# Kernel optimization log

Hardware: AMD Instinct MI355X
Metric: run time of the kernel (lower is better)

Reference implementation:

```python
import jax, jax.numpy as jnp
import numpy as np

B, C, H, W = 8, 512, 64, 64
RED = 4
CR = C // RED  # 128

def setup_inputs() -> dict:
    key = jax.random.key(0)
    k1, k2, k3 = jax.random.split(key, 3)
    x = jax.random.normal(k1, (B, C, H, W), dtype=jnp.float32)
    # conv_in: 1x1 conv, no bias -> weight [3*CR, C]
    w_in = jax.random.normal(k2, (3 * CR, C), dtype=jnp.float32) * 0.02
    # conv_out: 1x1 conv, no bias -> weight [C, CR]
    w_out = jax.random.normal(k3, (C, CR), dtype=jnp.float32) * 0.02
    return {"x": x, "w_in": w_in, "w_out": w_out}

def reference(x, w_in, w_out):
    b, c, h, w = x.shape
    n = h * w
    xf = x.reshape(b, c, n)                         # flatten spatial -> [B,C,N]
    proj = jnp.einsum('oc,bcn->bon', w_in, xf)      # 1x1 conv_in -> [B,3*CR,N]
    emb_a, emb_b, g = jnp.split(proj, 3, axis=1)    # each [B,CR,N]
    # unscaled full self-attention over N spatial tokens
    weights = jnp.einsum('bcn,bcm->bnm', emb_a, emb_b)   # [B,N,N]
    weights = jax.nn.softmax(weights, axis=2)
    y = jnp.einsum('bnm,bcm->bnc', weights, g)           # [B,N,CR]
    y = jnp.einsum('oc,bnc->bon', w_out, y)              # 1x1 conv_out -> [B,C,N]
    return x + y.reshape(b, c, h, w)
```

## Files before the change

### kernel.cpp

```cpp
#include <hip/hip_runtime.h>


typedef __attribute__((ext_vector_type(8))) short short8;
typedef __attribute__((ext_vector_type(4))) float f32x4;
typedef __attribute__((ext_vector_type(16))) float f32x16;

__device__ inline unsigned bfr(float f) {
  union { float f; unsigned u; } v; v.f = f;
  return v.u + 0x8000u;
}
__device__ inline unsigned short f2bf(float f) { return (unsigned short)(bfr(f) >> 16); }
__device__ inline unsigned pack2(float a, float b) {
  return __builtin_amdgcn_perm(bfr(b), bfr(a), 0x07060302u);
}
__device__ inline int sw(int row, int col, int stride_halves) {
  return row * stride_halves + ((((col >> 3) ^ (row & 7)) << 3) | (col & 7));
}
__device__ inline void load_lds16(const void* g, void* l) {
  __builtin_amdgcn_global_load_lds(
      (const __attribute__((address_space(1))) unsigned int*)g,
      (__attribute__((address_space(3))) unsigned int*)l, 16, 0, 0);
}

__global__ __launch_bounds__(256) void k_prep(const float* __restrict__ w_in,
                                              const float* __restrict__ w_out,
                                              unsigned short* __restrict__ wi,
                                              unsigned short* __restrict__ wo) {
  int i = blockIdx.x * 256 + threadIdx.x;
  const float* src;
  unsigned short* dst;
  int base;
  if (i < 24576) { src = w_in;  dst = wi; base = i * 8; }
  else           { src = w_out; dst = wo; base = (i - 24576) * 8; }
  float4 d0 = *(const float4*)&src[base];
  float4 d1 = *(const float4*)&src[base + 4];
  uint4 p;
  p.x = pack2(d0.x, d0.y); p.y = pack2(d0.z, d0.w);
  p.z = pack2(d1.x, d1.y); p.w = pack2(d1.z, d1.w);
  *(uint4*)&dst[base] = p;
}

__global__ __launch_bounds__(256) void k_proj(const float* __restrict__ x,
                                              const unsigned short* __restrict__ wi,
                                              unsigned short* __restrict__ ab,
                                              unsigned short* __restrict__ gC) {
  __shared__ unsigned short A_lds[128 * 64];
  __shared__ unsigned short B_lds[64 * 64];
  const int t = threadIdx.x;
  const int lane = t & 63;
  const int w = t >> 6;
  const int l15 = lane & 15;
  const int quad = lane >> 4;
  const int n0 = blockIdx.x * 64;
  const int o0 = blockIdx.y * 128;
  const int b = blockIdx.z;
  const int ch8g = t >> 5;
  const int tp = t & 31;

  f32x4 acc[2][4];
#pragma unroll
  for (int i = 0; i < 2; i++)
#pragma unroll
    for (int j = 0; j < 4; j++) acc[i][j] = (f32x4)0.f;

  for (int k0 = 0; k0 < 512; k0 += 64) {
#pragma unroll
    for (int j = 0; j < 4; j++) {
      int row = w * 32 + j * 8 + (lane >> 3);
      int gs = (lane & 7) ^ (row & 7);
      load_lds16(&wi[(size_t)(o0 + row) * 512 + k0 + gs * 8],
                 (void*)&A_lds[(w * 32 + j * 8) * 64]);
    }
    {
      float2 d[8];
#pragma unroll
      for (int j = 0; j < 8; j++)
        d[j] = *(const float2*)&x[((size_t)(b * 512 + k0 + ch8g * 8 + j)) * 4096 + n0 + tp * 2];
#pragma unroll
      for (int i = 0; i < 2; i++) {
        int r = tp * 2 + i;
        uint4 pv;
        if (i == 0) {
          pv.x = pack2(d[0].x, d[1].x); pv.y = pack2(d[2].x, d[3].x);
          pv.z = pack2(d[4].x, d[5].x); pv.w = pack2(d[6].x, d[7].x);
        } else {
          pv.x = pack2(d[0].y, d[1].y); pv.y = pack2(d[2].y, d[3].y);
          pv.z = pack2(d[4].y, d[5].y); pv.w = pack2(d[6].y, d[7].y);
        }
        *(uint4*)&B_lds[sw(r, ch8g * 8, 64)] = pv;
      }
    }
    __syncthreads();
#pragma unroll
    for (int kk = 0; kk < 64; kk += 32) {
      short8 a0 = *(const short8*)&A_lds[sw(w * 32 + l15, kk + quad * 8, 64)];
      short8 a1 = *(const short8*)&A_lds[sw(w * 32 + 16 + l15, kk + quad * 8, 64)];
#pragma unroll
      for (int ns = 0; ns < 4; ns++) {
        short8 bb = *(const short8*)&B_lds[sw(ns * 16 + l15, kk + quad * 8, 64)];
        acc[0][ns] = __builtin_amdgcn_mfma_f32_16x16x32_bf16(a0, bb, acc[0][ns], 0, 0, 0);
        acc[1][ns] = __builtin_amdgcn_mfma_f32_16x16x32_bf16(a1, bb, acc[1][ns], 0, 0, 0);
      }
    }
    __syncthreads();
  }
  if (o0 < 256) {
#pragma unroll
    for (int ms = 0; ms < 2; ms++) {
      int o = o0 + w * 32 + ms * 16 + quad * 4;
#pragma unroll
      for (int ns = 0; ns < 4; ns++) {
        int n = n0 + ns * 16 + l15;
        uint2 p;
        p.x = pack2(acc[ms][ns][0], acc[ms][ns][1]);
        p.y = pack2(acc[ms][ns][2], acc[ms][ns][3]);
        *(uint2*)&ab[((size_t)(b * 4096 + n)) * 256 + o] = p;
      }
    }
  } else {
#pragma unroll
    for (int ms = 0; ms < 2; ms++) {
      int og = w * 32 + ms * 16 + quad * 4;
#pragma unroll
      for (int ns = 0; ns < 4; ns++) {
        int n = n0 + ns * 16 + l15;
#pragma unroll
        for (int r = 0; r < 4; r++)
          gC[((size_t)(b * 128 + og + r)) * 4096 + n] = f2bf(acc[ms][ns][r]);
      }
    }
  }
}

__global__ __launch_bounds__(256, 2) void k_attn(const unsigned short* __restrict__ ab,
                                                 const unsigned short* __restrict__ gC,
                                                 unsigned short* __restrict__ yt) {
  __shared__ uint4 smem4[65536 / 16];
  unsigned short* smem_h = (unsigned short*)smem4;
  float* Obuf = (float*)smem4;
  float* lsumbuf = (float*)((char*)smem4 + 33024);
  unsigned* Pbuf = (unsigned*)((char*)smem4 + 33280);

  const int t = threadIdx.x;
  const int lane = t & 63;
  const int w = t >> 6;
  const int wr = w & 1;
  const int wc = w >> 1;
  const int l31 = lane & 31;
  const int h = lane >> 5;
  const int l7 = l31 & 7;
  const int q0 = blockIdx.x * 64;
  const int b = blockIdx.y;

  short8 qf[8];
  {
    const unsigned short* qp = &ab[((size_t)(b * 4096 + q0 + wc * 32 + l31)) * 256 + h * 8];
#pragma unroll
    for (int ks = 0; ks < 8; ks++) qf[ks] = *(const short8*)&qp[ks * 16];
  }

  const int krow_c = w * 16 + (lane >> 4);
  const int vrow_c = w * 32 + (lane >> 3);

  auto dma_tile = [&](int kt, int buf) {
    unsigned short* Kb = smem_h + buf * 8192;
    unsigned short* Vb = smem_h + 16384 + buf * 8192;
#pragma unroll
    for (int j = 0; j < 4; j++) {
      int row = krow_c + j * 4;
      int gs = (lane & 15) ^ (row & 7);
      load_lds16(&ab[((size_t)(b * 4096 + kt + row)) * 256 + 128 + gs * 8],
                 (void*)&Kb[(w * 16 + j * 4) * 128]);
    }
#pragma unroll
    for (int j = 0; j < 4; j++) {
      int row = vrow_c + j * 8;
      int gs = (lane & 7) ^ (row & 7);
      load_lds16(&gC[((size_t)(b * 128 + row)) * 4096 + kt + gs * 8],
                 (void*)&Vb[(w * 32 + j * 8) * 64]);
    }
  };

  f32x16 O[4];
#pragma unroll
  for (int i = 0; i < 4; i++) O[i] = (f32x16)0.f;
  float lsum = 0.f;
  const int rowK = wr * 32 + l31;

  dma_tile(0, 0);
  __syncthreads();

  for (int it = 0; it < 64; ++it) {
    if (it < 63) dma_tile((it + 1) * 64, (it + 1) & 1);
    const unsigned short* Kc = smem_h + (it & 1) * 8192;
    const unsigned short* Vc = smem_h + 16384 + (it & 1) * 8192;

    f32x16 accS = (f32x16)0.f;
#pragma unroll
    for (int ks = 0; ks < 8; ks++) {
      short8 ak = *(const short8*)&Kc[rowK * 128 + (((ks * 2 + h) ^ l7) << 3)];
      accS = __builtin_amdgcn_mfma_f32_32x32x16_bf16(ak, qf[ks], accS, 0, 0, 0);
    }

    float ps[16];
#pragma unroll
    for (int r = 0; r < 16; r++) {
      ps[r] = __expf(accS[r]);
      lsum += ps[r];
    }
    unsigned u[8];
#pragma unroll
    for (int i = 0; i < 8; i++) u[i] = pack2(ps[2 * i], ps[2 * i + 1]);

    short8 pfrag[2];
#pragma unroll
    for (int f = 0; f < 2; f++) {
      unsigned a0 = u[4 * f + 0], a1 = u[4 * f + 1], a2 = u[4 * f + 2], a3 = u[4 * f + 3];
      unsigned r0 = __shfl_xor(h ? a0 : a2, 32);
      unsigned r1 = __shfl_xor(h ? a1 : a3, 32);
      union { unsigned uu[4]; short8 s; } cv;
      if (h == 0) { cv.uu[0] = a0; cv.uu[1] = a1; cv.uu[2] = r0; cv.uu[3] = r1; }
      else        { cv.uu[0] = r0; cv.uu[1] = r1; cv.uu[2] = a2; cv.uu[3] = a3; }
      pfrag[f] = cv.s;
    }

#pragma unroll
    for (int ct = 0; ct < 4; ct++) {
      int rowV = ct * 32 + l31;
#pragma unroll
      for (int f = 0; f < 2; f++) {
        short8 av = *(const short8*)&Vc[rowV * 64 + (((wr * 4 + f * 2 + h) ^ l7) << 3)];
        O[ct] = __builtin_amdgcn_mfma_f32_32x32x16_bf16(av, pfrag[f], O[ct], 0, 0, 0);
      }
    }
    __syncthreads();
  }

  lsum += __shfl_xor(lsum, 32);
  const int q = wc * 32 + l31;
  if (wr == 0) {
#pragma unroll
    for (int ct = 0; ct < 4; ct++)
#pragma unroll
      for (int r = 0; r < 16; r++) {
        int c = ct * 32 + (r & 3) + 8 * (r >> 2) + 4 * h;
        Obuf[q * 129 + c] = O[ct][r];
      }
    if (h == 0) lsumbuf[q] = lsum;
  }
  __syncthreads();
  if (wr == 1) {
    float linv = 1.f / (lsum + lsumbuf[q]);
#pragma unroll
    for (int ct = 0; ct < 4; ct++)
#pragma unroll
      for (int r = 0; r < 16; r += 2) {
        int c = ct * 32 + (r & 3) + 8 * (r >> 2) + 4 * h;
        float v0 = (Obuf[q * 129 + c] + O[ct][r]) * linv;
        float v1 = (Obuf[q * 129 + c + 1] + O[ct][r + 1]) * linv;
        Pbuf[q * 65 + (c >> 1)] = pack2(v0, v1);
      }
  }
  __syncthreads();
  {
    int qq = t >> 2, seg = t & 3;
    unsigned* yrow = (unsigned*)&yt[((size_t)(b * 4096 + q0 + qq)) * 128];
#pragma unroll
    for (int i = 0; i < 4; i++) {
      uint4 v;
      v.x = Pbuf[qq * 65 + seg * 16 + i * 4 + 0];
      v.y = Pbuf[qq * 65 + seg * 16 + i * 4 + 1];
      v.z = Pbuf[qq * 65 + seg * 16 + i * 4 + 2];
      v.w = Pbuf[qq * 65 + seg * 16 + i * 4 + 3];
      *(uint4*)&yrow[seg * 16 + i * 4] = v;
    }
  }
}

__global__ __launch_bounds__(256) void k_out(const float* __restrict__ x,
                                             const unsigned short* __restrict__ wo,
                                             const unsigned short* __restrict__ yt,
                                             float* __restrict__ out) {
  __shared__ unsigned short A_lds[128 * 128];
  __shared__ unsigned short B_lds[64 * 128];
  const int t = threadIdx.x;
  const int lane = t & 63;
  const int w = t >> 6;
  const int l15 = lane & 15;
  const int quad = lane >> 4;
  const int n0 = blockIdx.x * 64;
  const int o0 = blockIdx.y * 128;
  const int b = blockIdx.z;

#pragma unroll
  for (int j = 0; j < 8; j++) {
    int row = w * 32 + j * 4 + (lane >> 4);
    int gs = (lane & 15) ^ (row & 7);
    load_lds16(&wo[(size_t)(o0 + row) * 128 + gs * 8],
               (void*)&A_lds[(w * 32 + j * 4) * 128]);
  }
#pragma unroll
  for (int j = 0; j < 4; j++) {
    int row = w * 16 + j * 4 + (lane >> 4);
    int gs = (lane & 15) ^ (row & 7);
    load_lds16(&yt[((size_t)(b * 4096 + n0 + row)) * 128 + gs * 8],
               (void*)&B_lds[(w * 16 + j * 4) * 128]);
  }
  __syncthreads();

  f32x4 acc[2][4];
#pragma unroll
  for (int i = 0; i < 2; i++)
#pragma unroll
    for (int j = 0; j < 4; j++) acc[i][j] = (f32x4)0.f;
#pragma unroll
  for (int ks = 0; ks < 4; ks++) {
    short8 a0 = *(const short8*)&A_lds[sw(w * 32 + l15, ks * 32 + quad * 8, 128)];
    short8 a1 = *(const short8*)&A_lds[sw(w * 32 + 16 + l15, ks * 32 + quad * 8, 128)];
#pragma unroll
    for (int ns = 0; ns < 4; ns++) {
      short8 bb = *(const short8*)&B_lds[sw(ns * 16 + l15, ks * 32 + quad * 8, 128)];
      acc[0][ns] = __builtin_amdgcn_mfma_f32_16x16x32_bf16(a0, bb, acc[0][ns], 0, 0, 0);
      acc[1][ns] = __builtin_amdgcn_mfma_f32_16x16x32_bf16(a1, bb, acc[1][ns], 0, 0, 0);
    }
  }
#pragma unroll
  for (int ms = 0; ms < 2; ms++) {
    int o = o0 + w * 32 + ms * 16 + quad * 4;
#pragma unroll
    for (int ns = 0; ns < 4; ns++) {
      int n = n0 + ns * 16 + l15;
#pragma unroll
      for (int r = 0; r < 4; r++) {
        size_t off = ((size_t)(b * 512 + o + r)) * 4096 + n;
        out[off] = x[off] + acc[ms][ns][r];
      }
    }
  }
}

extern "C" void kernel_launch(void* const* d_in, const int* in_sizes, int n_in,
                              void* d_out, int out_size, void* d_ws, size_t ws_size,
                              hipStream_t stream) {
  const float* x = (const float*)d_in[0];
  const float* w_in = (const float*)d_in[1];
  const float* w_out = (const float*)d_in[2];
  float* out = (float*)d_out;

  unsigned short* ab = (unsigned short*)d_ws;
  unsigned short* gC = ab + (size_t)8 * 4096 * 256;
  unsigned short* yt = gC + (size_t)8 * 128 * 4096;
  unsigned short* wi = yt + (size_t)8 * 4096 * 128;
  unsigned short* wo = wi + (size_t)384 * 512;

  k_prep<<<128, 256, 0, stream>>>(w_in, w_out, wi, wo);
  k_proj<<<dim3(64, 3, 8), 256, 0, stream>>>(x, wi, ab, gC);
  k_attn<<<dim3(64, 8), 256, 0, stream>>>(ab, gC, yt);
  k_out<<<dim3(64, 4, 8), 256, 0, stream>>>(x, wo, yt, out);
}
```

Before: 235.6 us.

## Pre-transpose x to bf16 token-major and pipeline projection GEMM with LDS DMA

Adds a kernel that converts x to bf16 and transposes it to [B,N,C]. The projection GEMM can then stream both operands with global_load_lds into double-buffered swizzled LDS tiles and use 32x32x16 MFMA. The goal is to drop the per-tile fp32 load, convert and transpose work inside the projection kernel and to overlap loads with compute. In exchange there is an extra kernel launch and an extra 32 MB round trip through memory. The old path is kept as a fallback when the workspace is too small.

New measurement: 250.0 us. 1.06x slower.

```diff
diff --git a/kernel.cpp b/kernel.cpp
--- a/kernel.cpp
+++ b/kernel.cpp
@@ -40,10 +40,132 @@
   *(uint4*)&dst[base] = p;
 }
 
-__global__ __launch_bounds__(256) void k_proj(const float* __restrict__ x,
+__global__ __launch_bounds__(256) void k_xpose(const float* __restrict__ x,
+                                               unsigned short* __restrict__ xbf) {
+  __shared__ unsigned short T[64 * 64];
+  const int t = threadIdx.x;
+  const int n0 = blockIdx.x * 64;
+  const int c0 = blockIdx.y * 64;
+  const int b = blockIdx.z;
+
+  float4 d[4];
+#pragma unroll
+  for (int j = 0; j < 4; j++) {
+    int c = c0 + (t >> 4) * 4 + j;
+    d[j] = *(const float4*)&x[((size_t)(b * 512 + c)) * 4096 + n0 + (t & 15) * 4];
+  }
+  const float* dp = (const float*)d;
+#pragma unroll
+  for (int i = 0; i < 4; i++) {
+    int n_loc = (t & 15) * 4 + i;
+    int c_loc = (t >> 4) * 4;
+    uint2 pv;
+    pv.x = pack2(dp[0 * 4 + i], dp[1 * 4 + i]);
+    pv.y = pack2(dp[2 * 4 + i], dp[3 * 4 + i]);
+    int pg = (c_loc >> 3) ^ ((n_loc >> 2) & 7);
+    *(uint2*)&T[n_loc * 64 + (pg << 3) + (c_loc & 7)] = pv;
+  }
+  __syncthreads();
+  {
+    int n = t >> 2, s = t & 3;
+    int x7 = (n >> 2) & 7;
+    uint4 lo = *(const uint4*)&T[n * 64 + (((2 * s + 0) ^ x7) << 3)];
+    uint4 hi = *(const uint4*)&T[n * 64 + (((2 * s + 1) ^ x7) << 3)];
+    unsigned short* dst = &xbf[((size_t)(b * 4096 + n0 + n)) * 512 + c0 + s * 16];
+    *(uint4*)&dst[0] = lo;
+    *(uint4*)&dst[8] = hi;
+  }
+}
+
+__global__ __launch_bounds__(256) void k_proj(const unsigned short* __restrict__ xbf,
                                               const unsigned short* __restrict__ wi,
                                               unsigned short* __restrict__ ab,
                                               unsigned short* __restrict__ gC) {
+  __shared__ unsigned short Abuf[2][128 * 64];
+  __shared__ unsigned short Bbuf[2][64 * 64];
+  const int t = threadIdx.x;
+  const int lane = t & 63;
+  const int w = t >> 6;
+  const int l31 = lane & 31;
+  const int h = lane >> 5;
+  const int n0 = blockIdx.x * 64;
+  const int o0 = blockIdx.y * 128;
+  const int b = blockIdx.z;
+
+  const int arow = w * 32 + (lane >> 3);
+  const int brow = w * 16 + (lane >> 3);
+
+  auto dma_tile = [&](int k0, int buf) {
+#pragma unroll
+    for (int j = 0; j < 4; j++) {
+      int row = arow + j * 8;
+      int gs = (lane & 7) ^ (row & 7);
+      load_lds16(&wi[(size_t)(o0 + row) * 512 + k0 + gs * 8],
+                 (void*)&Abuf[buf][(w * 32 + j * 8) * 64]);
+    }
+#pragma unroll
+    for (int j = 0; j < 2; j++) {
+      int row = brow + j * 8;
+      int gs = (lane & 7) ^ (row & 7);
+      load_lds16(&xbf[((size_t)(b * 4096 + n0 + row)) * 512 + k0 + gs * 8],
+                 (void*)&Bbuf[buf][(w * 16 + j * 8) * 64]);
+    }
+  };
+
+  f32x16 acc[2];
+  acc[0] = (f32x16)0.f;
+  acc[1] = (f32x16)0.f;
+
+  dma_tile(0, 0);
+  __syncthreads();
+
+  for (int it = 0; it < 8; ++it) {
+    if (it < 7) dma_tile((it + 1) * 64, (it + 1) & 1);
+    const unsigned short* A = Abuf[it & 1];
+    const unsigned short* Bm = Bbuf[it & 1];
+    short8 af[4];
+#pragma unroll
+    for (int ks = 0; ks < 4; ks++)
+      af[ks] = *(const short8*)&A[sw(w * 32 + l31, ks * 16 + h * 8, 64)];
+#pragma unroll
+    for (int nt = 0; nt < 2; nt++) {
+#pragma unroll
+      for (int ks = 0; ks < 4; ks++) {
+        short8 bf = *(const short8*)&Bm[sw(nt * 32 + l31, ks * 16 + h * 8, 64)];
+        acc[nt] = __builtin_amdgcn_mfma_f32_32x32x16_bf16(af[ks], bf, acc[nt], 0, 0, 0);
+      }
+    }
+    __syncthreads();
+  }
+
+  if (o0 < 256) {
+#pragma unroll
+    for (int nt = 0; nt < 2; nt++) {
+      int n = n0 + nt * 32 + l31;
+#pragma unroll
+      for (int r = 0; r < 16; r += 2) {
+        int o = o0 + w * 32 + (r & 3) + 8 * (r >> 2) + 4 * h;
+        *(unsigned*)&ab[((size_t)(b * 4096 + n)) * 256 + o] =
+            pack2(acc[nt][r], acc[nt][r + 1]);
+      }
+    }
+  } else {
+#pragma unroll
+    for (int nt = 0; nt < 2; nt++) {
+      int n = n0 + nt * 32 + l31;
+#pragma unroll
+      for (int r = 0; r < 16; r++) {
+        int c = w * 32 + (r & 3) + 8 * (r >> 2) + 4 * h;
+        gC[((size_t)(b * 128 + c)) * 4096 + n] = f2bf(acc[nt][r]);
+      }
+    }
+  }
+}
+
+__global__ __launch_bounds__(256) void k_proj_inline(const float* __restrict__ x,
+                                                     const unsigned short* __restrict__ wi,
+                                                     unsigned short* __restrict__ ab,
+                                                     unsigned short* __restrict__ gC) {
   __shared__ unsigned short A_lds[128 * 64];
   __shared__ unsigned short B_lds[64 * 64];
   const int t = threadIdx.x;
@@ -349,12 +471,22 @@
 
   unsigned short* ab = (unsigned short*)d_ws;
   unsigned short* gC = ab + (size_t)8 * 4096 * 256;
-  unsigned short* yt = gC + (size_t)8 * 128 * 4096;
-  unsigned short* wi = yt + (size_t)8 * 4096 * 128;
+  unsigned short* wi = gC + (size_t)8 * 128 * 4096;
   unsigned short* wo = wi + (size_t)384 * 512;
+  unsigned short* xbf = wo + (size_t)512 * 128;
+  const size_t need_big = (size_t)(8388608 + 4194304 + 196608 + 65536 + 16777216) * 2;
 
   k_prep<<<128, 256, 0, stream>>>(w_in, w_out, wi, wo);
-  k_proj<<<dim3(64, 3, 8), 256, 0, stream>>>(x, wi, ab, gC);
-  k_attn<<<dim3(64, 8), 256, 0, stream>>>(ab, gC, yt);
-  k_out<<<dim3(64, 4, 8), 256, 0, stream>>>(x, wo, yt, out);
-}
+  if (ws_size >= need_big) {
+    unsigned short* yt = xbf;
+    k_xpose<<<dim3(64, 8, 8), 256, 0, stream>>>(x, xbf);
+    k_proj<<<dim3(64, 3, 8), 256, 0, stream>>>(xbf, wi, ab, gC);
+    k_attn<<<dim3(64, 8), 256, 0, stream>>>(ab, gC, yt);
+    k_out<<<dim3(64, 4, 8), 256, 0, stream>>>(x, wo, yt, out);
+  } else {
+    unsigned short* yt = xbf;
+    k_proj_inline<<<dim3(64, 3, 8), 256, 0, stream>>>(x, wi, ab, gC);
+    k_attn<<<dim3(64, 8), 256, 0, stream>>>(ab, gC, yt);
+    k_out<<<dim3(64, 4, 8), 256, 0, stream>>>(x, wo, yt, out);
+  }
+}
```
